# Kernel tuning notes

Measured on AMD Instinct MI355X. Metric: run time of the kernel, lower is better.

The kernel has to match this reference:

```python
import jax, jax.numpy as jnp
import numpy as np

B, S, HID, NH, FF, K = 2, 2048, 1024, 16, 4096, 512
DH = HID // NH


def setup_inputs() -> dict:
    key = jax.random.key(0)
    ks = jax.random.split(key, 24)
    w = lambda k, shape: (jax.random.normal(k, shape, jnp.float32) * 0.02)
    inp = {
        'x': jax.random.normal(ks[0], (B, S, HID), jnp.float32),
        'mask': jnp.ones((B, 1, 1, S), jnp.int32),
        'Wq': w(ks[1], (HID, HID)), 'bq': jnp.zeros((HID,), jnp.float32),
        'Wk': w(ks[2], (HID, HID)), 'bk': jnp.zeros((HID,), jnp.float32),
        'Wv': w(ks[3], (HID, HID)), 'bv': jnp.zeros((HID,), jnp.float32),
        'Wo': w(ks[4], (HID, HID)), 'bo': jnp.zeros((HID,), jnp.float32),
        'rel_emb': w(ks[5], (2 * K, HID)),
        'Wpk': w(ks[6], (HID, HID)), 'bpk': jnp.zeros((HID,), jnp.float32),
        'Wpq': w(ks[7], (HID, HID)), 'bpq': jnp.zeros((HID,), jnp.float32),
        'ln1_g': jnp.ones((HID,), jnp.float32), 'ln1_b': jnp.zeros((HID,), jnp.float32),
        'ln2_g': jnp.ones((HID,), jnp.float32), 'ln2_b': jnp.zeros((HID,), jnp.float32),
        'W1': w(ks[8], (HID, FF)), 'b1': jnp.zeros((FF,), jnp.float32),
        'W2': w(ks[9], (FF, HID)), 'b2': jnp.zeros((HID,), jnp.float32),
    }
    return inp


def _layernorm(x, g, b, eps=1e-6):
    m = jnp.mean(x, -1, keepdims=True)
    v = jnp.mean(jnp.square(x - m), -1, keepdims=True)
    return (x - m) * jax.lax.rsqrt(v + eps) * g + b


def _disentangled_attention(x, mask, Wq, bq, Wk, bk, Wv, bv, Wo, bo,
                            rel_emb, Wpk, bpk, Wpq, bpq):
    # content projections -> [B, NH, S, DH]
    def heads(t):
        return t.reshape(B, S, NH, DH).transpose(0, 2, 1, 3)
    q = heads(x @ Wq + bq)
    k = heads(x @ Wk + bk)
    v = heads(x @ Wv + bv)

    # relative position index: rel[i, j] = clip(i - j, -K, K-1) + K in [0, 2K)
    pos = jnp.arange(S)
    rel = jnp.clip(pos[:, None] - pos[None, :], -K, K - 1) + K  # [S, S]

    # projected relative-position embeddings -> [2K, NH, DH]
    pos_k = (rel_emb @ Wpk + bpk).reshape(2 * K, NH, DH)
    pos_q = (rel_emb @ Wpq + bpq).reshape(2 * K, NH, DH)

    # content-to-content
    c2c = jnp.einsum('bhid,bhjd->bhij', q, k)
    # content-to-position: gather over relative bucket per (i, j)
    c2p_att = jnp.einsum('bhid,rhd->bhir', q, pos_k)               # [B,NH,S,2K]
    c2p = jnp.take_along_axis(c2p_att, rel[None, None, :, :], axis=-1)
    # position-to-content: K_j . Q_r[delta(j, i)], gather then transpose
    p2c_att = jnp.einsum('bhjd,rhd->bhjr', k, pos_q)               # [B,NH,S,2K]
    p2c = jnp.take_along_axis(p2c_att, rel[None, None, :, :], axis=-1)
    p2c = p2c.transpose(0, 1, 3, 2)

    scale = 1.0 / jnp.sqrt(jnp.asarray(3 * DH, jnp.float32))
    scores = (c2c + c2p + p2c) * scale                             # [B,NH,S,S]
    scores = jnp.where(mask == 0, jnp.asarray(-1e9, scores.dtype), scores)
    attn = jax.nn.softmax(scores, axis=-1)

    out = jnp.einsum('bhij,bhjd->bhid', attn, v)
    out = out.transpose(0, 2, 1, 3).reshape(B, S, HID)
    return out @ Wo + bo


def reference(x, mask, Wq, bq, Wk, bk, Wv, bv, Wo, bo, rel_emb, Wpk, bpk,
              Wpq, bpq, ln1_g, ln1_b, ln2_g, ln2_b, W1, b1, W2, b2):
    # pre-norm sublayer 1: x + attn(LN(x))
    h = x + _disentangled_attention(_layernorm(x, ln1_g, ln1_b), mask,
                                    Wq, bq, Wk, bk, Wv, bv, Wo, bo,
                                    rel_emb, Wpk, bpk, Wpq, bpq)
    # pre-norm sublayer 2: h + FFN(LN(h)), GELU activation
    hn = _layernorm(h, ln2_g, ln2_b)
    ff = jax.nn.gelu(hn @ W1 + b1) @ W2 + b2
    return h + ff
```

## Files before the change

### kernel.cpp

```cpp
#include <hip/hip_runtime.h>
#include <cstdint>
#include <cstddef>

#define DEV __device__ __forceinline__

typedef __attribute__((ext_vector_type(4))) float  f32x4;
typedef __attribute__((ext_vector_type(4))) float  float4v;
typedef __attribute__((ext_vector_type(8))) short  s16x8;
typedef __attribute__((ext_vector_type(4))) short  s16x4;

static constexpr int BB = 2, SS = 2048, HIDN = 1024, NHH = 16, FFN = 4096, DH = 64;
static constexpr int TWOK = 1024;
static constexpr int HG = 8;
static constexpr float ATT_SCALE = 0.07216878364870322f;

DEV short f2bf(float f) {
  union { float f; uint32_t u; } v; v.f = f;
  uint32_t r = (v.u + 0x7fffu + ((v.u >> 16) & 1u)) >> 16;
  return (short)r;
}
DEV float bfu(unsigned short u) {
  union { uint32_t u; float f; } v; v.u = ((uint32_t)u) << 16; return v.f;
}
DEV int imin(int a, int b) { return a < b ? a : b; }
DEV int imax(int a, int b) { return a > b ? a : b; }

DEV void gl_lds16(const void* g, void* l) {
  __builtin_amdgcn_global_load_lds((const __attribute__((address_space(1))) void*)g,
                                   (__attribute__((address_space(3))) void*)l, 16, 0, 0);
}

#define MFMA16(a, b, c) __builtin_amdgcn_mfma_f32_16x16x32_bf16((a), (b), (c), 0, 0, 0)

__global__ __launch_bounds__(256) void k_tcast(const float* __restrict__ in,
                                               short* __restrict__ out, int R, int C) {
  __shared__ float t[32][33];
  const int bx = blockIdx.x * 32, by = blockIdx.y * 32;
  const int tx = threadIdx.x & 31, ty = threadIdx.x >> 5;
#pragma unroll
  for (int r = ty; r < 32; r += 8) t[r][tx] = in[(size_t)(by + r) * C + bx + tx];
  __syncthreads();
#pragma unroll
  for (int c = ty; c < 32; c += 8) out[(size_t)(bx + c) * R + by + tx] = f2bf(t[tx][c]);
}

struct TCBatch { const float* in[5]; short* out[5]; };
__global__ __launch_bounds__(256) void k_tcast5(TCBatch tc) {
  __shared__ float t[32][33];
  const float* in = tc.in[blockIdx.z];
  short* out = tc.out[blockIdx.z];
  const int bx = blockIdx.x * 32, by = blockIdx.y * 32;
  const int tx = threadIdx.x & 31, ty = threadIdx.x >> 5;
#pragma unroll
  for (int r = ty; r < 32; r += 8) t[r][tx] = in[(size_t)(by + r) * 1024 + bx + tx];
  __syncthreads();
#pragma unroll
  for (int c = ty; c < 32; c += 8) out[(size_t)(bx + c) * 1024 + by + tx] = f2bf(t[tx][c]);
}

__global__ __launch_bounds__(256) void k_cast(const float* __restrict__ in,
                                              short* __restrict__ out, int n4) {
  const int i = blockIdx.x * 256 + threadIdx.x;
  if (i < n4) {
    float4v v = ((const float4v*)in)[i];
    s16x4 o; o[0] = f2bf(v.x); o[1] = f2bf(v.y); o[2] = f2bf(v.z); o[3] = f2bf(v.w);
    ((s16x4*)out)[i] = o;
  }
}

__global__ __launch_bounds__(256) void k_ln(const float* __restrict__ x,
                                            const float* __restrict__ gw,
                                            const float* __restrict__ bw,
                                            short* __restrict__ out) {
  const int row = blockIdx.x, t = threadIdx.x, lane = t & 63, wv = t >> 6;
  __shared__ float red[8];
  const float4v v = ((const float4v*)(x + (size_t)row * HIDN))[t];
  float s = v.x + v.y + v.z + v.w;
#pragma unroll
  for (int d = 1; d < 64; d <<= 1) s += __shfl_xor(s, d, 64);
  if (lane == 0) red[wv] = s;
  __syncthreads();
  const float mean = (red[0] + red[1] + red[2] + red[3]) * (1.f / 1024.f);
  const float dx = v.x - mean, dy = v.y - mean, dz = v.z - mean, dw = v.w - mean;
  float s2 = dx * dx + dy * dy + dz * dz + dw * dw;
#pragma unroll
  for (int d = 1; d < 64; d <<= 1) s2 += __shfl_xor(s2, d, 64);
  if (lane == 0) red[4 + wv] = s2;
  __syncthreads();
  const float var = (red[4] + red[5] + red[6] + red[7]) * (1.f / 1024.f);
  const float rs = rsqrtf(var + 1e-6f);
  const float4v g4 = ((const float4v*)gw)[t], b4 = ((const float4v*)bw)[t];
  s16x4 o;
  o[0] = f2bf(dx * rs * g4.x + b4.x);
  o[1] = f2bf(dy * rs * g4.y + b4.y);
  o[2] = f2bf(dz * rs * g4.z + b4.z);
  o[3] = f2bf(dw * rs * g4.w + b4.w);
  ((s16x4*)(out + (size_t)row * HIDN))[t] = o;
}

DEV void gemm_main(const short* __restrict__ A, const short* __restrict__ Bt, int K,
                   int m0, int n0, int tid, int wm, int wn, int lr, int lg,
                   short* As, short* Bs, f32x4 acc[4][4]) {
  for (int k0 = 0; k0 < K; k0 += 32) {
#pragma unroll
    for (int c = tid; c < 512; c += 256) {
      const int row = c >> 2, col = (c & 3) * 8;
      gl_lds16(A + (size_t)(m0 + row) * K + k0 + col, (char*)As + c * 16);
      gl_lds16(Bt + (size_t)(n0 + row) * K + k0 + col, (char*)Bs + c * 16);
    }
    __syncthreads();
    s16x8 af[4], bf[4];
#pragma unroll
    for (int fi = 0; fi < 4; ++fi) af[fi] = *(const s16x8*)&As[(wm + fi * 16 + lr) * 32 + lg * 8];
#pragma unroll
    for (int fj = 0; fj < 4; ++fj) bf[fj] = *(const s16x8*)&Bs[(wn + fj * 16 + lr) * 32 + lg * 8];
#pragma unroll
    for (int fi = 0; fi < 4; ++fi)
#pragma unroll
      for (int fj = 0; fj < 4; ++fj) acc[fi][fj] = MFMA16(af[fi], bf[fj], acc[fi][fj]);
    __syncthreads();
  }
}

enum { OM_GELU = 0, OM_RESID = 1 };

template <int OM>
__global__ __launch_bounds__(256) void k_gemm(const short* __restrict__ A,
                                              const short* __restrict__ Bt,
                                              const float* __restrict__ bias,
                                              const float* __restrict__ resid,
                                              void* __restrict__ out,
                                              int M, int N, int K) {
  __shared__ short As[128 * 32];
  __shared__ short Bs[128 * 32];
  const int tid = threadIdx.x, lane = tid & 63, wave = tid >> 6;
  const int m0 = blockIdx.y * 128, n0 = blockIdx.x * 128;
  const int wm = (wave >> 1) * 64, wn = (wave & 1) * 64;
  const int lr = lane & 15, lg = lane >> 4;

  f32x4 acc[4][4];
#pragma unroll
  for (int i = 0; i < 4; ++i)
#pragma unroll
    for (int j = 0; j < 4; ++j) acc[i][j] = (f32x4){0.f, 0.f, 0.f, 0.f};
  gemm_main(A, Bt, K, m0, n0, tid, wm, wn, lr, lg, As, Bs, acc);

#pragma unroll
  for (int fi = 0; fi < 4; ++fi)
#pragma unroll
    for (int fj = 0; fj < 4; ++fj) {
      const int n = n0 + wn + fj * 16 + lr;
      const float bv = bias[n];
#pragma unroll
      for (int r = 0; r < 4; ++r) {
        const int m = m0 + wm + fi * 16 + lg * 4 + r;
        float v = acc[fi][fj][r] + bv;
        if constexpr (OM == OM_GELU) {
          const float z = 0.7978845608028654f * (v + 0.044715f * v * v * v);
          const float th = 1.f - 2.f / (1.f + __expf(2.f * z));
          ((short*)out)[(size_t)m * N + n] = f2bf(0.5f * v * (1.f + th));
        } else {
          ((float*)out)[(size_t)m * N + n] = v + resid[(size_t)m * N + n];
        }
      }
    }
}

__global__ __launch_bounds__(256) void k_gemm_qkv(const short* __restrict__ A,
                                                  const short* __restrict__ Bt,
                                                  const float* __restrict__ bq,
                                                  const float* __restrict__ bk,
                                                  const float* __restrict__ bv,
                                                  short* __restrict__ qo,
                                                  short* __restrict__ ko,
                                                  short* __restrict__ vo) {
  __shared__ short As[128 * 32];
  __shared__ short Bs[128 * 32];
  const int tid = threadIdx.x, lane = tid & 63, wave = tid >> 6;
  const int m0 = blockIdx.y * 128, n0 = blockIdx.x * 128;
  const int wm = (wave >> 1) * 64, wn = (wave & 1) * 64;
  const int lr = lane & 15, lg = lane >> 4;

  f32x4 acc[4][4];
#pragma unroll
  for (int i = 0; i < 4; ++i)
#pragma unroll
    for (int j = 0; j < 4; ++j) acc[i][j] = (f32x4){0.f, 0.f, 0.f, 0.f};
  gemm_main(A, Bt, 1024, m0, n0, tid, wm, wn, lr, lg, As, Bs, acc);

#pragma unroll
  for (int fi = 0; fi < 4; ++fi)
#pragma unroll
    for (int fj = 0; fj < 4; ++fj) {
      const int n = n0 + wn + fj * 16 + lr;
      const int proj = n >> 10, nn = n & 1023;
      const int hh = nn >> 6, dd = nn & 63;
      const float bvv = (proj == 0 ? bq : proj == 1 ? bk : bv)[nn];
#pragma unroll
      for (int r = 0; r < 4; ++r) {
        const int m = m0 + wm + fi * 16 + lg * 4 + r;
        const int b = m >> 11, s = m & (SS - 1);
        const float v = acc[fi][fj][r] + bvv;
        if (proj == 2)
          vo[(((size_t)b * NHH + hh) * DH + dd) * SS + s] = f2bf(v);
        else
          (proj == 0 ? qo : ko)[(((size_t)b * NHH + hh) * SS + s) * DH + dd] = f2bf(v);
      }
    }
}

__global__ __launch_bounds__(256) void k_gemm_pos(const short* __restrict__ A,
                                                  const short* __restrict__ Bt,
                                                  const float* __restrict__ bpk,
                                                  const float* __restrict__ bpq,
                                                  short* __restrict__ pko,
                                                  short* __restrict__ pqo) {
  __shared__ short As[128 * 32];
  __shared__ short Bs[128 * 32];
  const int tid = threadIdx.x, lane = tid & 63, wave = tid >> 6;
  const int m0 = blockIdx.y * 128, n0 = blockIdx.x * 128;
  const int wm = (wave >> 1) * 64, wn = (wave & 1) * 64;
  const int lr = lane & 15, lg = lane >> 4;

  f32x4 acc[4][4];
#pragma unroll
  for (int i = 0; i < 4; ++i)
#pragma unroll
    for (int j = 0; j < 4; ++j) acc[i][j] = (f32x4){0.f, 0.f, 0.f, 0.f};
  gemm_main(A, Bt, 1024, m0, n0, tid, wm, wn, lr, lg, As, Bs, acc);

#pragma unroll
  for (int fi = 0; fi < 4; ++fi)
#pragma unroll
    for (int fj = 0; fj < 4; ++fj) {
      const int n = n0 + wn + fj * 16 + lr;
      const int pos = n >> 10, nn = n & 1023;
      const int hh = nn >> 6, dd = nn & 63;
      const float bvv = (pos == 0 ? bpk : bpq)[nn];
      short* ob = pos == 0 ? pko : pqo;
#pragma unroll
      for (int r = 0; r < 4; ++r) {
        const int m = m0 + wm + fi * 16 + lg * 4 + r;
        ob[((size_t)hh * TWOK + m) * DH + dd] = f2bf(acc[fi][fj][r] + bvv);
      }
    }
}

__global__ __launch_bounds__(256) void k_posgemm(const short* __restrict__ qh,
                                                 const short* __restrict__ kh,
                                                 const short* __restrict__ posk,
                                                 const short* __restrict__ posq,
                                                 short* __restrict__ c2pO,
                                                 short* __restrict__ p2cO,
                                                 short* __restrict__ p2cE, int h0) {
  __shared__ short As[128 * 64];
  __shared__ short Bs[128 * 64];
  const int tid = threadIdx.x, lane = tid & 63, wave = tid >> 6;
  const int z = blockIdx.z;
  const int hl = z & (HG - 1), b = (z >> 3) & 1, isP = z >> 4;
  const int h = h0 + hl;
  const int bhl = b * HG + hl;
  const int m0 = blockIdx.y * 128, n0 = blockIdx.x * 128;
  const int wm = (wave >> 1) * 64, wn = (wave & 1) * 64;
  const int lr = lane & 15, lg = lane >> 4;
  const short* Ab = (isP ? kh : qh) + ((size_t)b * NHH + h) * SS * DH;
  const short* Pb = (isP ? posq : posk) + (size_t)h * TWOK * DH;
  short* ob = (isP ? p2cO : c2pO) + (size_t)bhl * SS * TWOK;

#pragma unroll
  for (int c = tid; c < 1024; c += 256) {
    const int row = c >> 3, col = (c & 7) * 8;
    gl_lds16(Ab + (size_t)(m0 + row) * DH + col, (char*)As + c * 16);
    gl_lds16(Pb + (size_t)(n0 + row) * DH + col, (char*)Bs + c * 16);
  }
  __syncthreads();

  f32x4 acc[4][4];
#pragma unroll
  for (int i = 0; i < 4; ++i)
#pragma unroll
    for (int j = 0; j < 4; ++j) acc[i][j] = (f32x4){0.f, 0.f, 0.f, 0.f};

#pragma unroll
  for (int ks = 0; ks < 2; ++ks) {
    s16x8 af[4], bf[4];
#pragma unroll
    for (int fi = 0; fi < 4; ++fi) af[fi] = *(const s16x8*)&As[(wm + fi * 16 + lr) * 64 + ks * 32 + lg * 8];
#pragma unroll
    for (int fj = 0; fj < 4; ++fj) bf[fj] = *(const s16x8*)&Bs[(wn + fj * 16 + lr) * 64 + ks * 32 + lg * 8];
#pragma unroll
    for (int fi = 0; fi < 4; ++fi)
#pragma unroll
      for (int fj = 0; fj < 4; ++fj) acc[fi][fj] = MFMA16(af[fi], bf[fj], acc[fi][fj]);
  }

#pragma unroll
  for (int fi = 0; fi < 4; ++fi)
#pragma unroll
    for (int fj = 0; fj < 4; ++fj) {
      const int n = n0 + wn + fj * 16 + lr;
#pragma unroll
      for (int r = 0; r < 4; ++r) {
        const int m = m0 + wm + fi * 16 + lg * 4 + r;
        const short val = f2bf(acc[fi][fj][r]);
        ob[(size_t)m * TWOK + n] = val;
        if (isP) {
          if (n == 0)        p2cE[((size_t)bhl * 2 + 0) * SS + m] = val;
          if (n == TWOK - 1) p2cE[((size_t)bhl * 2 + 1) * SS + m] = val;
        }
      }
    }
}

__global__ __launch_bounds__(512) void k_attn(const short* __restrict__ qh,
                                              const short* __restrict__ kh,
                                              const short* __restrict__ vT,
                                              const short* __restrict__ c2p,
                                              const short* __restrict__ p2c,
                                              const short* __restrict__ p2cE,
                                              const int* __restrict__ mask,
                                              short* __restrict__ ao, int h0) {
  __shared__ char smem[8 * 16 * 68 * 4];
  __shared__ float Mm[8][16];
  __shared__ float Lm[8][16];
  float (*Om)[16][68] = (float(*)[16][68])smem;
  short (*Ps)[16][72] = (short(*)[16][72])smem;

  const int tid = threadIdx.x, lane = tid & 63, wv = tid >> 6;
  const int lr = lane & 15, lg = lane >> 4;

  const int bid = blockIdx.x;
  const int itile = bid & 127;
  const int hl = (bid >> 7) & (HG - 1);
  const int b = bid >> 10;
  const int h = h0 + hl;
  const int i0 = itile * 16;
  const size_t bhoff = ((size_t)b * NHH + h) * SS * DH;
  const size_t bhl = (size_t)b * HG + hl;
  const int jq0 = wv * (SS / 8);

  const short* qrow = qh + bhoff + (size_t)(i0 + lr) * DH + lg * 8;
  const s16x8 qa0 = *(const s16x8*)qrow;
  const s16x8 qa1 = *(const s16x8*)(qrow + 32);

  const unsigned short* c2prow[4];
  float cLoV[4], cHiV[4];
#pragma unroll
  for (int r = 0; r < 4; ++r) {
    c2prow[r] = (const unsigned short*)(c2p + (bhl * SS + (size_t)(i0 + lg * 4 + r)) * TWOK);
    cLoV[r] = bfu(c2prow[r][0]);
    cHiV[r] = bfu(c2prow[r][TWOK - 1]);
  }
  const unsigned short* p2cb = (const unsigned short*)(p2c + bhl * SS * TWOK);
  const unsigned short* pE0 = (const unsigned short*)(p2cE + (bhl * 2 + 0) * SS);
  const unsigned short* pE1 = (const unsigned short*)(p2cE + (bhl * 2 + 1) * SS);

  const int dbase = i0 + lg * 4 - lr;

  f32x4 oacc[4];
  float mprev[4], lsum[4];
#pragma unroll
  for (int r = 0; r < 4; ++r) {
    mprev[r] = -1e30f; lsum[r] = 0.f; oacc[r] = (f32x4){0.f, 0.f, 0.f, 0.f};
  }

  for (int jt = 0; jt < SS / 8 / 64; ++jt) {
    const int j0 = jq0 + jt * 64;
    const int d0 = i0 - j0;

    f32x4 sacc[4];
#pragma unroll
    for (int fj = 0; fj < 4; ++fj) {
      const short* krow = kh + bhoff + (size_t)(j0 + fj * 16 + lr) * DH + lg * 8;
      const s16x8 k0 = *(const s16x8*)krow;
      const s16x8 k1 = *(const s16x8*)(krow + 32);
      f32x4 a = (f32x4){0.f, 0.f, 0.f, 0.f};
      a = MFMA16(qa0, k0, a);
      a = MFMA16(qa1, k1, a);
      sacc[fj] = a;
    }

    float pvv[4][4];
    if (d0 >= 576) {
#pragma unroll
      for (int fj = 0; fj < 4; ++fj) {
        const int jl = fj * 16 + lr;
        const bool ok = mask[(size_t)b * SS + j0 + jl] != 0;
        const float pe = bfu(pE0[j0 + jl]);
#pragma unroll
        for (int r = 0; r < 4; ++r) {
          const float s = (sacc[fj][r] + cHiV[r] + pe) * ATT_SCALE;
          pvv[fj][r] = ok ? s : -1e9f;
        }
      }
    } else if (d0 <= -528) {
#pragma unroll
      for (int fj = 0; fj < 4; ++fj) {
        const int jl = fj * 16 + lr;
        const bool ok = mask[(size_t)b * SS + j0 + jl] != 0;
        const float pe = bfu(pE1[j0 + jl]);
#pragma unroll
        for (int r = 0; r < 4; ++r) {
          const float s = (sacc[fj][r] + cLoV[r] + pe) * ATT_SCALE;
          pvv[fj][r] = ok ? s : -1e9f;
        }
      }
    } else {
#pragma unroll
      for (int fj = 0; fj < 4; ++fj) {
        const int jl = fj * 16 + lr;
        const bool ok = mask[(size_t)b * SS + j0 + jl] != 0;
        const unsigned short* prow = p2cb + (size_t)(j0 + jl) * TWOK;
        const int dl0 = dbase - fj * 16 - j0;
#pragma unroll
        for (int r = 0; r < 4; ++r) {
          const int dl = dl0 + r;
          const int cc = imin(imax(dl + 512, 0), 1023);
          const int cp = imin(imax(512 - dl, 0), 1023);
          const float s = (sacc[fj][r] + bfu(c2prow[r][cc]) + bfu(prow[cp])) * ATT_SCALE;
          pvv[fj][r] = ok ? s : -1e9f;
        }
      }
    }

#pragma unroll
    for (int r = 0; r < 4; ++r) {
      float m = fmaxf(fmaxf(pvv[0][r], pvv[1][r]), fmaxf(pvv[2][r], pvv[3][r]));
#pragma unroll
      for (int dd = 1; dd < 16; dd <<= 1) m = fmaxf(m, __shfl_xor(m, dd, 64));
      const float mnew = fmaxf(mprev[r], m);
      const float corr = __expf(mprev[r] - mnew);
      float rs = 0.f;
#pragma unroll
      for (int fj = 0; fj < 4; ++fj) { pvv[fj][r] = __expf(pvv[fj][r] - mnew); rs += pvv[fj][r]; }
#pragma unroll
      for (int dd = 1; dd < 16; dd <<= 1) rs += __shfl_xor(rs, dd, 64);
      lsum[r] = lsum[r] * corr + rs;
      mprev[r] = mnew;
#pragma unroll
      for (int fd = 0; fd < 4; ++fd) oacc[fd][r] *= corr;
    }

#pragma unroll
    for (int fj = 0; fj < 4; ++fj)
#pragma unroll
      for (int r = 0; r < 4; ++r)
        Ps[wv][lg * 4 + r][fj * 16 + lr] = f2bf(pvv[fj][r]);

    const s16x8 pa0 = *(const s16x8*)&Ps[wv][lr][lg * 8];
    const s16x8 pa1 = *(const s16x8*)&Ps[wv][lr][32 + lg * 8];
#pragma unroll
    for (int fd = 0; fd < 4; ++fd) {
      const short* vrow = vT + bhoff + (size_t)(fd * 16 + lr) * SS + j0 + lg * 8;
      const s16x8 v0 = *(const s16x8*)vrow;
      const s16x8 v1 = *(const s16x8*)(vrow + 32);
      oacc[fd] = MFMA16(pa0, v0, oacc[fd]);
      oacc[fd] = MFMA16(pa1, v1, oacc[fd]);
    }
  }

  __syncthreads();
#pragma unroll
  for (int fd = 0; fd < 4; ++fd)
#pragma unroll
    for (int r = 0; r < 4; ++r)
      Om[wv][lg * 4 + r][fd * 16 + lr] = oacc[fd][r];
  if (lr == 0) {
#pragma unroll
    for (int r = 0; r < 4; ++r) { Mm[wv][lg * 4 + r] = mprev[r]; Lm[wv][lg * 4 + r] = lsum[r]; }
  }
  __syncthreads();

  if (wv < 4) {
#pragma unroll
    for (int r = 0; r < 4; ++r) {
      const int il = lg * 4 + r;
      float mt = -1e30f;
#pragma unroll
      for (int w = 0; w < 8; ++w) mt = fmaxf(mt, Mm[w][il]);
      float L = 0.f, o = 0.f;
#pragma unroll
      for (int w = 0; w < 8; ++w) {
        const float sc = __expf(Mm[w][il] - mt);
        L += Lm[w][il] * sc;
        o += Om[w][il][wv * 16 + lr] * sc;
      }
      ao[((size_t)b * SS + i0 + il) * HIDN + h * DH + wv * 16 + lr] = f2bf(o / L);
    }
  }
}

extern "C" void kernel_launch(void* const* d_in, const int* in_sizes, int n_in,
                              void* d_out, int out_size, void* d_ws, size_t ws_size,
                              hipStream_t stream) {
  const float* x   = (const float*)d_in[0];
  const int* mask  = (const int*)d_in[1];
  const float* Wq  = (const float*)d_in[2];  const float* bq  = (const float*)d_in[3];
  const float* Wk  = (const float*)d_in[4];  const float* bk  = (const float*)d_in[5];
  const float* Wv  = (const float*)d_in[6];  const float* bv  = (const float*)d_in[7];
  const float* Wo  = (const float*)d_in[8];  const float* bo  = (const float*)d_in[9];
  const float* rel = (const float*)d_in[10];
  const float* Wpk = (const float*)d_in[11]; const float* bpk = (const float*)d_in[12];
  const float* Wpq = (const float*)d_in[13]; const float* bpq = (const float*)d_in[14];
  const float* g1  = (const float*)d_in[15]; const float* be1 = (const float*)d_in[16];
  const float* g2  = (const float*)d_in[17]; const float* be2 = (const float*)d_in[18];
  const float* W1  = (const float*)d_in[19]; const float* bf1 = (const float*)d_in[20];
  const float* W2  = (const float*)d_in[21]; const float* bf2 = (const float*)d_in[22];
  float* out = (float*)d_out;

  char* ws = (char*)d_ws;
  const size_t MB = (size_t)1 << 20;
  short* aoB   = (short*)(ws + 0 * MB);
  short* qhB   = (short*)(ws + 8 * MB);
  short* khB   = (short*)(ws + 16 * MB);
  short* vTB   = (short*)(ws + 24 * MB);
  short* poskB = (short*)(ws + 32 * MB);
  short* posqB = (short*)(ws + 34 * MB);
  short* xn    = (short*)(ws + 36 * MB);
  short* WqT   = (short*)(ws + 44 * MB);
  short* WkT   = (short*)(ws + 46 * MB);
  short* WvT   = (short*)(ws + 48 * MB);
  short* WpkT  = (short*)(ws + 50 * MB);
  short* WpqT  = (short*)(ws + 52 * MB);
  short* relbf = (short*)(ws + 54 * MB);
  short* c2pG  = (short*)(ws + 36 * MB);
  short* p2cG  = (short*)(ws + 100 * MB);
  short* p2cE  = (short*)(ws + 164 * MB);
  short* WoT   = (short*)(ws + 36 * MB);
  short* hnB   = (short*)(ws + 38 * MB);
  short* W1T   = (short*)(ws + 46 * MB);
  short* W2T   = (short*)(ws + 54 * MB);
  short* midB  = (short*)(ws + 62 * MB);
  (void)ws_size; (void)in_sizes; (void)n_in; (void)out_size;

  const int M = BB * SS;

  TCBatch tc;
  tc.in[0] = Wq;  tc.out[0] = WqT;
  tc.in[1] = Wk;  tc.out[1] = WkT;
  tc.in[2] = Wv;  tc.out[2] = WvT;
  tc.in[3] = Wpk; tc.out[3] = WpkT;
  tc.in[4] = Wpq; tc.out[4] = WpqT;
  k_tcast5<<<dim3(32, 32, 5), 256, 0, stream>>>(tc);
  k_cast<<<1024, 256, 0, stream>>>(rel, relbf, 1024 * 1024 / 4);
  k_ln<<<M, 256, 0, stream>>>(x, g1, be1, xn);

  k_gemm_qkv<<<dim3(24, 32), 256, 0, stream>>>(xn, WqT, bq, bk, bv, qhB, khB, vTB);
  k_gemm_pos<<<dim3(16, 8), 256, 0, stream>>>(relbf, WpkT, bpk, bpq, poskB, posqB);

  for (int g = 0; g < NHH / HG; ++g) {
    const int h0 = g * HG;
    k_posgemm<<<dim3(8, 16, 4 * HG), 256, 0, stream>>>(qhB, khB, poskB, posqB,
                                                       c2pG, p2cG, p2cE, h0);
    k_attn<<<BB * HG * 128, 512, 0, stream>>>(qhB, khB, vTB, c2pG, p2cG, p2cE, mask, aoB, h0);
  }

  k_tcast<<<dim3(32, 32), 256, 0, stream>>>(Wo, WoT, 1024, 1024);
  k_gemm<OM_RESID><<<dim3(8, 32), 256, 0, stream>>>(aoB, WoT, bo, x, out, M, 1024, 1024);
  k_ln<<<M, 256, 0, stream>>>(out, g2, be2, hnB);
  k_tcast<<<dim3(128, 32), 256, 0, stream>>>(W1, W1T, 1024, 4096);
  k_tcast<<<dim3(32, 128), 256, 0, stream>>>(W2, W2T, 4096, 1024);
  k_gemm<OM_GELU><<<dim3(32, 32), 256, 0, stream>>>(hnB, W1T, bf1, nullptr, midB, M, 4096, 1024);
  k_gemm<OM_RESID><<<dim3(8, 32), 256, 0, stream>>>(midB, W2T, bf2, out, out, M, 1024, 4096);
}
```

Measured before the change: 672.8 us.

## Stage c2p rows and mask in LDS, transpose score MFMA for per-lane row softmax

Each attention block now loads its 16 c2p rows and the batch mask into LDS once, using global_load_lds, so the inner loop no longer gathers them from global memory. The QK MFMA operands are swapped so each lane holds one query row. The online softmax then reduces with two cross-lane shuffles per tile instead of a 16-lane reduction per row, and P is written to LDS as packed 4-element stores. The cost is about 75 KB of dynamic LDS per block, which limits how many blocks fit on a CU, plus an extra barrier after the upfront load.

```diff
diff --git a/kernel.cpp b/kernel.cpp
--- a/kernel.cpp
+++ b/kernel.cpp
@@ -13,6 +13,12 @@
 static constexpr int TWOK = 1024;
 static constexpr int HG = 8;
 static constexpr float ATT_SCALE = 0.07216878364870322f;
+
+static constexpr int ROWB = 2056;
+static constexpr int OFF_C2P = 0;
+static constexpr int OFF_MSK = 32896;
+static constexpr int OFF_OVL = 41088;
+static constexpr int DYN_LDS = 75904;
 
 DEV short f2bf(float f) {
   union { float f; uint32_t u; } v; v.f = f;
@@ -320,11 +326,13 @@
                                               const short* __restrict__ p2cE,
                                               const int* __restrict__ mask,
                                               short* __restrict__ ao, int h0) {
-  __shared__ char smem[8 * 16 * 68 * 4];
+  extern __shared__ char dynL[];
+  char* c2pL = dynL + OFF_C2P;
+  const int* maskL = (const int*)(dynL + OFF_MSK);
+  float (*Om)[16][68] = (float(*)[16][68])(dynL + OFF_OVL);
+  short (*Ps)[16][72] = (short(*)[16][72])(dynL + OFF_OVL);
   __shared__ float Mm[8][16];
   __shared__ float Lm[8][16];
-  float (*Om)[16][68] = (float(*)[16][68])smem;
-  short (*Ps)[16][72] = (short(*)[16][72])smem;
 
   const int tid = threadIdx.x, lane = tid & 63, wv = tid >> 6;
   const int lr = lane & 15, lg = lane >> 4;
@@ -339,30 +347,29 @@
   const size_t bhl = (size_t)b * HG + hl;
   const int jq0 = wv * (SS / 8);
 
+  for (int u = tid; u < 2048; u += 512) {
+    const int ri = u >> 7, off = (u & 127) * 16;
+    gl_lds16((const char*)(c2p + (bhl * SS + (size_t)(i0 + ri)) * TWOK) + off,
+             c2pL + ri * ROWB + off);
+  }
+  gl_lds16((const char*)(mask + (size_t)b * SS) + tid * 16, (char*)(dynL + OFF_MSK) + tid * 16);
+
   const short* qrow = qh + bhoff + (size_t)(i0 + lr) * DH + lg * 8;
   const s16x8 qa0 = *(const s16x8*)qrow;
   const s16x8 qa1 = *(const s16x8*)(qrow + 32);
 
-  const unsigned short* c2prow[4];
-  float cLoV[4], cHiV[4];
-#pragma unroll
-  for (int r = 0; r < 4; ++r) {
-    c2prow[r] = (const unsigned short*)(c2p + (bhl * SS + (size_t)(i0 + lg * 4 + r)) * TWOK);
-    cLoV[r] = bfu(c2prow[r][0]);
-    cHiV[r] = bfu(c2prow[r][TWOK - 1]);
-  }
+  __syncthreads();
+
+  const float cLo = bfu(*(const unsigned short*)(c2pL + lr * ROWB));
+  const float cHi = bfu(*(const unsigned short*)(c2pL + lr * ROWB + (TWOK - 1) * 2));
   const unsigned short* p2cb = (const unsigned short*)(p2c + bhl * SS * TWOK);
   const unsigned short* pE0 = (const unsigned short*)(p2cE + (bhl * 2 + 0) * SS);
   const unsigned short* pE1 = (const unsigned short*)(p2cE + (bhl * 2 + 1) * SS);
 
-  const int dbase = i0 + lg * 4 - lr;
-
   f32x4 oacc[4];
-  float mprev[4], lsum[4];
-#pragma unroll
-  for (int r = 0; r < 4; ++r) {
-    mprev[r] = -1e30f; lsum[r] = 0.f; oacc[r] = (f32x4){0.f, 0.f, 0.f, 0.f};
-  }
+  float mrow = -1e30f, lrow = 0.f;
+#pragma unroll
+  for (int r = 0; r < 4; ++r) oacc[r] = (f32x4){0.f, 0.f, 0.f, 0.f};
 
   for (int jt = 0; jt < SS / 8 / 64; ++jt) {
     const int j0 = jq0 + jt * 64;
@@ -375,77 +382,85 @@
       const s16x8 k0 = *(const s16x8*)krow;
       const s16x8 k1 = *(const s16x8*)(krow + 32);
       f32x4 a = (f32x4){0.f, 0.f, 0.f, 0.f};
-      a = MFMA16(qa0, k0, a);
-      a = MFMA16(qa1, k1, a);
+      a = MFMA16(k0, qa0, a);
+      a = MFMA16(k1, qa1, a);
       sacc[fj] = a;
     }
 
+    const int jbase = j0 + lg * 4;
     float pvv[4][4];
     if (d0 >= 576) {
 #pragma unroll
-      for (int fj = 0; fj < 4; ++fj) {
-        const int jl = fj * 16 + lr;
-        const bool ok = mask[(size_t)b * SS + j0 + jl] != 0;
-        const float pe = bfu(pE0[j0 + jl]);
+      for (int fj = 0; fj < 4; ++fj)
 #pragma unroll
         for (int r = 0; r < 4; ++r) {
-          const float s = (sacc[fj][r] + cHiV[r] + pe) * ATT_SCALE;
+          const int jb = jbase + fj * 16 + r;
+          const bool ok = maskL[jb] != 0;
+          const float s = (sacc[fj][r] + cHi + bfu(pE0[jb])) * ATT_SCALE;
           pvv[fj][r] = ok ? s : -1e9f;
         }
-      }
     } else if (d0 <= -528) {
 #pragma unroll
-      for (int fj = 0; fj < 4; ++fj) {
-        const int jl = fj * 16 + lr;
-        const bool ok = mask[(size_t)b * SS + j0 + jl] != 0;
-        const float pe = bfu(pE1[j0 + jl]);
+      for (int fj = 0; fj < 4; ++fj)
 #pragma unroll
         for (int r = 0; r < 4; ++r) {
-          const float s = (sacc[fj][r] + cLoV[r] + pe) * ATT_SCALE;
+          const int jb = jbase + fj * 16 + r;
+          const bool ok = maskL[jb] != 0;
+          const float s = (sacc[fj][r] + cLo + bfu(pE1[jb])) * ATT_SCALE;
           pvv[fj][r] = ok ? s : -1e9f;
         }
-      }
     } else {
-#pragma unroll
-      for (int fj = 0; fj < 4; ++fj) {
-        const int jl = fj * 16 + lr;
-        const bool ok = mask[(size_t)b * SS + j0 + jl] != 0;
-        const unsigned short* prow = p2cb + (size_t)(j0 + jl) * TWOK;
-        const int dl0 = dbase - fj * 16 - j0;
+      const int ii = i0 + lr;
+#pragma unroll
+      for (int fj = 0; fj < 4; ++fj)
 #pragma unroll
         for (int r = 0; r < 4; ++r) {
-          const int dl = dl0 + r;
+          const int jb = jbase + fj * 16 + r;
+          const bool ok = maskL[jb] != 0;
+          const int dl = ii - jb;
           const int cc = imin(imax(dl + 512, 0), 1023);
           const int cp = imin(imax(512 - dl, 0), 1023);
-          const float s = (sacc[fj][r] + bfu(c2prow[r][cc]) + bfu(prow[cp])) * ATT_SCALE;
+          const float c2pv = bfu(*(const unsigned short*)(c2pL + lr * ROWB + cc * 2));
+          const float p2cv = bfu(p2cb[(size_t)jb * TWOK + cp]);
+          const float s = (sacc[fj][r] + c2pv + p2cv) * ATT_SCALE;
           pvv[fj][r] = ok ? s : -1e9f;
         }
-      }
-    }
-
-#pragma unroll
-    for (int r = 0; r < 4; ++r) {
-      float m = fmaxf(fmaxf(pvv[0][r], pvv[1][r]), fmaxf(pvv[2][r], pvv[3][r]));
-#pragma unroll
-      for (int dd = 1; dd < 16; dd <<= 1) m = fmaxf(m, __shfl_xor(m, dd, 64));
-      const float mnew = fmaxf(mprev[r], m);
-      const float corr = __expf(mprev[r] - mnew);
-      float rs = 0.f;
-#pragma unroll
-      for (int fj = 0; fj < 4; ++fj) { pvv[fj][r] = __expf(pvv[fj][r] - mnew); rs += pvv[fj][r]; }
-#pragma unroll
-      for (int dd = 1; dd < 16; dd <<= 1) rs += __shfl_xor(rs, dd, 64);
-      lsum[r] = lsum[r] * corr + rs;
-      mprev[r] = mnew;
-#pragma unroll
-      for (int fd = 0; fd < 4; ++fd) oacc[fd][r] *= corr;
-    }
-
+    }
+
+    float mx = pvv[0][0];
 #pragma unroll
     for (int fj = 0; fj < 4; ++fj)
 #pragma unroll
-      for (int r = 0; r < 4; ++r)
-        Ps[wv][lg * 4 + r][fj * 16 + lr] = f2bf(pvv[fj][r]);
+      for (int r = 0; r < 4; ++r) mx = fmaxf(mx, pvv[fj][r]);
+    mx = fmaxf(mx, __shfl_xor(mx, 16, 64));
+    mx = fmaxf(mx, __shfl_xor(mx, 32, 64));
+    const float mnew = fmaxf(mrow, mx);
+    const float corr = __expf(mrow - mnew);
+    float sm = 0.f;
+#pragma unroll
+    for (int fj = 0; fj < 4; ++fj)
+#pragma unroll
+      for (int r = 0; r < 4; ++r) { pvv[fj][r] = __expf(pvv[fj][r] - mnew); sm += pvv[fj][r]; }
+    sm += __shfl_xor(sm, 16, 64);
+    sm += __shfl_xor(sm, 32, 64);
+    lrow = lrow * corr + sm;
+    mrow = mnew;
+
+    float corr4[4];
+#pragma unroll
+    for (int r = 0; r < 4; ++r) corr4[r] = __shfl(corr, lg * 4 + r, 64);
+#pragma unroll
+    for (int fd = 0; fd < 4; ++fd)
+#pragma unroll
+      for (int r = 0; r < 4; ++r) oacc[fd][r] *= corr4[r];
+
+#pragma unroll
+    for (int fj = 0; fj < 4; ++fj) {
+      s16x4 pw;
+#pragma unroll
+      for (int r = 0; r < 4; ++r) pw[r] = f2bf(pvv[fj][r]);
+      *(s16x4*)&Ps[wv][lr][fj * 16 + lg * 4] = pw;
+    }
 
     const s16x8 pa0 = *(const s16x8*)&Ps[wv][lr][lg * 8];
     const s16x8 pa1 = *(const s16x8*)&Ps[wv][lr][32 + lg * 8];
@@ -465,10 +480,7 @@
 #pragma unroll
     for (int r = 0; r < 4; ++r)
       Om[wv][lg * 4 + r][fd * 16 + lr] = oacc[fd][r];
-  if (lr == 0) {
-#pragma unroll
-    for (int r = 0; r < 4; ++r) { Mm[wv][lg * 4 + r] = mprev[r]; Lm[wv][lg * 4 + r] = lsum[r]; }
-  }
+  if (lg == 0) { Mm[wv][lr] = mrow; Lm[wv][lr] = lrow; }
   __syncthreads();
 
   if (wv < 4) {
@@ -552,7 +564,8 @@
     const int h0 = g * HG;
     k_posgemm<<<dim3(8, 16, 4 * HG), 256, 0, stream>>>(qhB, khB, poskB, posqB,
                                                        c2pG, p2cG, p2cE, h0);
-    k_attn<<<BB * HG * 128, 512, 0, stream>>>(qhB, khB, vTB, c2pG, p2cG, p2cE, mask, aoB, h0);
+    k_attn<<<BB * HG * 128, 512, DYN_LDS, stream>>>(qhB, khB, vTB, c2pG, p2cG, p2cE,
+                                                    mask, aoB, h0);
   }
 
   k_tcast<<<dim3(32, 32), 256, 0, stream>>>(Wo, WoT, 1024, 1024);
```

Result: faster. 605.0 us (-10.1%).
